# Performance work log

Measured on AMD Instinct MI355X. Metric: run time of the kernel, lower is better.

Reference implementation:

```python
import jax, jax.numpy as jnp
import numpy as np

Q, N, S, A, E, H = 2048, 64, 128, 4, 128, 8
D = E // H
NEG = -1e9

def _mlp(x, w1, b1, w2, b2):
    return jax.nn.silu(x @ w1 + b1) @ w2 + b2

def _mha(x, wq, bq, wk, bk, wv, bv, wo, bo):
    # MultiHeadAttention with default activation=relu applied to q,k,v and output
    q = jax.nn.relu(x @ wq + bq)
    k = jax.nn.relu(x @ wk + bk)
    v = jax.nn.relu(x @ wv + bv)
    def split(t):
        return t.reshape(Q, N, H, D).transpose(0, 2, 1, 3)  # [Q,H,N,D]
    qh, kh, vh = split(q), split(k), split(v)
    scores = jnp.einsum('bhqd,bhkd->bhqk', qh, kh) / (D ** 0.5)
    attn = jax.nn.softmax(scores, axis=-1)
    y = jnp.einsum('bhqk,bhkd->bhqd', attn, vh).transpose(0, 2, 1, 3).reshape(Q, N, E)
    return jax.nn.relu(y @ wo + bo)

def setup_inputs():
    key = jax.random.key(0)
    ks = jax.random.split(key, 26)
    nrm = lambda k, s: jax.random.normal(k, s, jnp.float32) * 0.05
    return {
        'tasks': jax.random.normal(ks[0], (Q, N, N + 4 * S), jnp.float32),
        'constraints': jax.random.normal(ks[1], (Q, A), jnp.float32),
        'masks': jax.random.randint(ks[2], (Q, N, S), 0, 2),
        'topologicals': jax.random.randint(ks[3], (Q, N), 0, N),
        'w_init1': nrm(ks[4], (N + A, 128)), 'b_init1': jnp.zeros((128,), jnp.float32),
        'w_init2': nrm(ks[5], (128, E)), 'b_init2': jnp.zeros((E,), jnp.float32),
        'wq': nrm(ks[6], (E, E)), 'bq': jnp.zeros((E,), jnp.float32),
        'wk': nrm(ks[7], (E, E)), 'bk': jnp.zeros((E,), jnp.float32),
        'wv': nrm(ks[8], (E, E)), 'bv': jnp.zeros((E,), jnp.float32),
        'wo': nrm(ks[9], (E, E)), 'bo': jnp.zeros((E,), jnp.float32),
        'w_node1': nrm(ks[10], (E + A, 128)), 'b_node1': jnp.zeros((128,), jnp.float32),
        'w_node2': nrm(ks[11], (128, E)), 'b_node2': jnp.zeros((E,), jnp.float32),
        'w_ser1': nrm(ks[12], (A, 128)), 'b_ser1': jnp.zeros((128,), jnp.float32),
        'w_ser2': nrm(ks[13], (128, E)), 'b_ser2': jnp.zeros((E,), jnp.float32),
    }

def reference(tasks, constraints, masks, topologicals,
              w_init1, b_init1, w_init2, b_init2,
              wq, bq, wk, bk, wv, bv, wo, bo,
              w_node1, b_node1, w_node2, b_node2,
              w_ser1, b_ser1, w_ser2, b_ser2):
    cons = jnp.broadcast_to(constraints[:, None, :], (Q, N, A))
    node_emb = _mlp(jnp.concatenate([tasks[:, :, :N], cons], -1), w_init1, b_init1, w_init2, b_init2)
    nodes_emb = _mha(node_emb, wq, bq, wk, bk, wv, bv, wo, bo) + node_emb
    # original sets channel 0 to -3 then overwrites with 3; channel 2 stays 0 (kept faithfully)
    qos = jnp.zeros((Q, N, A), jnp.float32).at[:, :, 0].set(3.0).at[:, :, 1].set(1.0).at[:, :, 3].set(1.0)
    ava = jnp.ones((Q,), jnp.float32)
    tp = jnp.full((Q,), 3.0, jnp.float32)
    rel = jnp.ones((Q,), jnp.float32)
    ridx = jnp.zeros((Q, N), jnp.float32)
    rprob = jnp.zeros((Q, N), jnp.float32)
    qidx = jnp.arange(Q)
    topo_seq = topologicals[:, ::-1].T  # [N, Q]: reversed topological order, one node per step
    keys = jax.random.split(jax.random.key(1), N)

    def step(carry, xs):
        qos, ava, tp, rel, ridx, rprob = carry
        topo, k = xs
        task = tasks[qidx, topo]                 # [Q, N + 4S] per-query gathered row
        workflow = task[:, :N]
        response_time = jnp.max(workflow * qos[:, :, 0], axis=1)  # [Q]
        qos_feat = jnp.stack([response_time, ava, tp, rel], axis=-1)
        node_e = nodes_emb[qidx, topo]           # [Q, E]
        tne = _mlp(jnp.concatenate([node_e, qos_feat], -1), w_node1, b_node1, w_node2, b_node2)
        services = task[:, N:].reshape(Q, S, A)
        ser_emb = _mlp(services, w_ser1, b_ser1, w_ser2, b_ser2)
        logits = jnp.einsum('qse,qe->qs', ser_emb, tne)
        mask = masks[qidx, topo]                 # [Q, S]
        logits = jnp.where(mask == 0, NEG, logits)
        ser_prob = jax.nn.softmax(logits, axis=-1)
        ser_idx = jax.random.categorical(k, logits)  # ~ Categorical(ser_prob)
        onehot = jax.nn.one_hot(topo, N, dtype=jnp.float32)
        ridx = ridx + onehot * ser_idx[:, None].astype(jnp.float32)
        rprob = rprob + onehot * ser_prob[qidx, ser_idx][:, None]
        base = ser_idx * 4 + N
        ser_rt = task[qidx, base]
        ser_ava = task[qidx, base + 1]
        ser_tp = task[qidx, base + 2]
        ser_rel = task[qidx, base + 3]
        new_tp = jnp.minimum(ser_tp, tp)
        qos = qos.at[qidx, topo, 0].set(ser_rt + response_time)
        qos = qos.at[qidx, topo, 1].set(ser_ava * ava)
        qos = qos.at[qidx, topo, 2].set(new_tp)
        qos = qos.at[qidx, topo, 3].set(ser_rel * rel)
        return (qos, ser_ava * ava, new_tp, ser_rel * rel, ridx, rprob), None

    (qos, ava, tp, rel, ridx, rprob), _ = jax.lax.scan(
        step, (qos, ava, tp, rel, ridx, rprob), (topo_seq, keys))
    return ridx.astype(jnp.int16), rprob
```

## Files before the change

### kernel.cpp

```cpp
#include <hip/hip_runtime.h>
#include <math.h>

#define Qn 2048
#define Nn 64
#define Sn 128
#define An 4
#define En 128
#define TASKW 576
#define NEGV -1000000000.0f

typedef float v2f __attribute__((ext_vector_type(2)));
typedef float v4f __attribute__((ext_vector_type(4)));

__device__ __forceinline__ v2f mkv2(float a, float b) {
  v2f r; r.x = a; r.y = b; return r;
}
__device__ __forceinline__ v2f lo2(v4f v) { v2f r; r.x = v.x; r.y = v.y; return r; }
__device__ __forceinline__ v2f hi2(v4f v) { v2f r; r.x = v.z; r.y = v.w; return r; }
__device__ __forceinline__ void pkfma(v2f& d, v2f a, v2f b) {
  asm("v_pk_fma_f32 %0, %1, %2, %0" : "+v"(d) : "v"(a), "v"(b));
}
__device__ __forceinline__ v2f pkadd(v2f a, v2f b) {
  v2f d; asm("v_pk_add_f32 %0, %1, %2" : "=v"(d) : "v"(a), "v"(b)); return d;
}

__device__ __forceinline__ void threefry2x32(unsigned k0, unsigned k1,
                                             unsigned x0, unsigned x1,
                                             unsigned& o0, unsigned& o1) {
  unsigned ks2 = k0 ^ k1 ^ 0x1BD11BDAu;
  x0 += k0; x1 += k1;
#define TFR(r) { x0 += x1; x1 = (x1 << (r)) | (x1 >> (32 - (r))); x1 ^= x0; }
  TFR(13) TFR(15) TFR(26) TFR(6)
  x0 += k1;  x1 += ks2 + 1u;
  TFR(17) TFR(29) TFR(16) TFR(24)
  x0 += ks2; x1 += k0 + 2u;
  TFR(13) TFR(15) TFR(26) TFR(6)
  x0 += k0;  x1 += k1 + 3u;
  TFR(17) TFR(29) TFR(16) TFR(24)
  x0 += k1;  x1 += ks2 + 4u;
  TFR(13) TFR(15) TFR(26) TFR(6)
  x0 += ks2; x1 += k0 + 5u;
#undef TFR
  o0 = x0; o1 = x1;
}

__device__ __forceinline__ float silu_f(float x) {
  return x / (1.0f + expf(-x));
}
__device__ __forceinline__ float fexp(float x) {
  return __builtin_amdgcn_exp2f(x * 1.44269504088896f);
}
__device__ __forceinline__ float fsilu(float x) {
  const float e = __builtin_amdgcn_exp2f(x * -1.44269504088896f);
  return x * __builtin_amdgcn_rcpf(1.0f + e);
}
__device__ __forceinline__ float flog(float x) {
  return __builtin_amdgcn_logf(x) * 0.69314718055995f;
}

__global__ void setup_kernel(const float* __restrict__ w_node2,
                             const float* __restrict__ b_node2,
                             const float* __restrict__ w_ser2,
                             const float* __restrict__ b_ser2,
                             float* __restrict__ Mbuf, float* __restrict__ dvec,
                             unsigned* __restrict__ keys) {
  const int b = blockIdx.x, t = threadIdx.x;
  if (b < 128) {
    float acc = 0.0f;
    for (int e = 0; e < 128; ++e)
      acc = fmaf(w_node2[b * 128 + e], w_ser2[t * 128 + e], acc);
    Mbuf[b * 128 + t] = acc;
  } else if (b == 128) {
    float acc = 0.0f;
    for (int e = 0; e < 128; ++e)
      acc = fmaf(b_node2[e], w_ser2[t * 128 + e], acc);
    dvec[t] = acc;
  } else {
    if (t < 64) {
      unsigned o0, o1;
      threefry2x32(0u, 1u, 0u, (unsigned)t, o0, o1);
      keys[2 * t + 0] = o0;
      keys[2 * t + 1] = o1;
    }
  }
}

__global__ __launch_bounds__(256, 2)
void init_mlp_kernel(const float* __restrict__ tasks,
                     const float* __restrict__ cons,
                     const float* __restrict__ w1, const float* __restrict__ b1,
                     const float* __restrict__ w2, const float* __restrict__ b2,
                     float* __restrict__ node_emb) {
  const int q = blockIdx.x, tid = threadIdx.x;
  const int lane = tid & 127, half = tid >> 7;
  __shared__ __align__(16) float xr[2][68];
  __shared__ __align__(16) float sgb[2][128];
  v2f w1p[34], w2p[64];
#pragma unroll
  for (int i = 0; i < 34; ++i)
    w1p[i] = mkv2(w1[(2 * i) * 128 + lane], w1[(2 * i + 1) * 128 + lane]);
#pragma unroll
  for (int j = 0; j < 64; ++j)
    w2p[j] = mkv2(w2[(2 * j) * 128 + lane], w2[(2 * j + 1) * 128 + lane]);
  const float bb1 = b1[lane], bb2 = b2[lane];
  for (int r = 0; r < 64; r += 2) {
    if (tid < 136) {
      const int rr = tid / 68, j = tid - rr * 68;
      xr[rr][j] = (j < 64) ? tasks[(q * 64 + r + rr) * TASKW + j]
                           : cons[q * 4 + (j - 64)];
    }
    __syncthreads();
    v2f gp = mkv2(0.0f, 0.0f);
    const v4f* xr4 = (const v4f*)&xr[half][0];
#pragma unroll
    for (int i = 0; i < 17; ++i) {
      const v4f x = xr4[i];
      pkfma(gp, lo2(x), w1p[2 * i]);
      pkfma(gp, hi2(x), w1p[2 * i + 1]);
    }
    const float g = gp.x + gp.y + bb1;
    sgb[half][lane] = silu_f(g);
    __syncthreads();
    v2f op = mkv2(0.0f, 0.0f);
    const v4f* sgb4 = (const v4f*)&sgb[half][0];
#pragma unroll
    for (int j = 0; j < 32; ++j) {
      const v4f s = sgb4[j];
      pkfma(op, lo2(s), w2p[2 * j]);
      pkfma(op, hi2(s), w2p[2 * j + 1]);
    }
    node_emb[(q * 64 + r + half) * 128 + lane] = op.x + op.y + bb2;
    __syncthreads();
  }
}

__global__ __launch_bounds__(256, 2)
void mha_kernel(const float* __restrict__ node_emb,
                const float* __restrict__ wq, const float* __restrict__ bq,
                const float* __restrict__ wk, const float* __restrict__ bk,
                const float* __restrict__ wv, const float* __restrict__ bv,
                float* __restrict__ y_out) {
  const int q = blockIdx.x, tid = threadIdx.x;
  __shared__ __align__(16) float xs[64][132];
  __shared__ __align__(16) float qh[64][20];
  __shared__ __align__(16) float kh[64][20];
  __shared__ __align__(16) float vt[16][68];
  __shared__ __align__(16) float pool[3 * 16 * 132];
  float (*wht)[16][132] = (float (*)[16][132])pool;
  float (*at)[68] = (float (*)[68])pool;

  for (int idx = tid; idx < 64 * 32; idx += 256) {
    const int n = idx >> 5, e4 = idx & 31;
    *(v4f*)&xs[n][4 * e4] =
        *(const v4f*)&node_emb[(q * 64 + n) * 128 + 4 * e4];
  }
  __syncthreads();

  const int d16 = tid >> 4;
  const int ng = tid & 15;

  for (int hd = 0; hd < 8; ++hd) {
    for (int idx = tid; idx < 3 * 128 * 16; idx += 256) {
      const int m = idx >> 11, k = (idx >> 4) & 127, d = idx & 15;
      const float* W = (m == 0) ? wq : (m == 1) ? wk : wv;
      wht[m][d][k] = W[k * 128 + hd * 16 + d];
    }
    __syncthreads();

    {
      const float bqv = bq[hd * 16 + d16];
      const float bkv = bk[hd * 16 + d16];
      const float bvv = bv[hd * 16 + d16];
      const v4f* wq4 = (const v4f*)&wht[0][d16][0];
      const v4f* wk4 = (const v4f*)&wht[1][d16][0];
      const v4f* wv4 = (const v4f*)&wht[2][d16][0];
      const v4f* xr0 = (const v4f*)&xs[ng][0];
      const v4f* xr1 = (const v4f*)&xs[ng + 16][0];
      const v4f* xr2 = (const v4f*)&xs[ng + 32][0];
      const v4f* xr3 = (const v4f*)&xs[ng + 48][0];
      v2f aq0 = mkv2(0, 0), aq1 = mkv2(0, 0), aq2 = mkv2(0, 0), aq3 = mkv2(0, 0);
      v2f ak0 = mkv2(0, 0), ak1 = mkv2(0, 0), ak2 = mkv2(0, 0), ak3 = mkv2(0, 0);
      v2f av0 = mkv2(0, 0), av1 = mkv2(0, 0), av2 = mkv2(0, 0), av3 = mkv2(0, 0);
#pragma unroll 4
      for (int kk = 0; kk < 32; ++kk) {
        const v4f wqv = wq4[kk], wkv = wk4[kk], wvv = wv4[kk];
        const v4f x0 = xr0[kk], x1 = xr1[kk], x2 = xr2[kk], x3 = xr3[kk];
        const v2f wqa = lo2(wqv), wqb = hi2(wqv);
        const v2f wka = lo2(wkv), wkb = hi2(wkv);
        const v2f wva = lo2(wvv), wvb = hi2(wvv);
        const v2f x0a = lo2(x0), x0b = hi2(x0);
        const v2f x1a = lo2(x1), x1b = hi2(x1);
        const v2f x2a = lo2(x2), x2b = hi2(x2);
        const v2f x3a = lo2(x3), x3b = hi2(x3);
        pkfma(aq0, x0a, wqa); pkfma(aq0, x0b, wqb);
        pkfma(aq1, x1a, wqa); pkfma(aq1, x1b, wqb);
        pkfma(aq2, x2a, wqa); pkfma(aq2, x2b, wqb);
        pkfma(aq3, x3a, wqa); pkfma(aq3, x3b, wqb);
        pkfma(ak0, x0a, wka); pkfma(ak0, x0b, wkb);
        pkfma(ak1, x1a, wka); pkfma(ak1, x1b, wkb);
        pkfma(ak2, x2a, wka); pkfma(ak2, x2b, wkb);
        pkfma(ak3, x3a, wka); pkfma(ak3, x3b, wkb);
        pkfma(av0, x0a, wva); pkfma(av0, x0b, wvb);
        pkfma(av1, x1a, wva); pkfma(av1, x1b, wvb);
        pkfma(av2, x2a, wva); pkfma(av2, x2b, wvb);
        pkfma(av3, x3a, wva); pkfma(av3, x3b, wvb);
      }
      qh[ng][d16] = fmaxf(aq0.x + aq0.y + bqv, 0.0f);
      qh[ng + 16][d16] = fmaxf(aq1.x + aq1.y + bqv, 0.0f);
      qh[ng + 32][d16] = fmaxf(aq2.x + aq2.y + bqv, 0.0f);
      qh[ng + 48][d16] = fmaxf(aq3.x + aq3.y + bqv, 0.0f);
      kh[ng][d16] = fmaxf(ak0.x + ak0.y + bkv, 0.0f);
      kh[ng + 16][d16] = fmaxf(ak1.x + ak1.y + bkv, 0.0f);
      kh[ng + 32][d16] = fmaxf(ak2.x + ak2.y + bkv, 0.0f);
      kh[ng + 48][d16] = fmaxf(ak3.x + ak3.y + bkv, 0.0f);
      vt[d16][ng] = fmaxf(av0.x + av0.y + bvv, 0.0f);
      vt[d16][ng + 16] = fmaxf(av1.x + av1.y + bvv, 0.0f);
      vt[d16][ng + 32] = fmaxf(av2.x + av2.y + bvv, 0.0f);
      vt[d16][ng + 48] = fmaxf(av3.x + av3.y + bvv, 0.0f);
    }
    __syncthreads();

    {
      const int n = tid >> 2, mg = tid & 3;
      v4f qv[4];
      const v4f* qrow = (const v4f*)&qh[n][0];
#pragma unroll
      for (int kk = 0; kk < 4; ++kk) qv[kk] = qrow[kk];
#pragma unroll 4
      for (int jj = 0; jj < 16; ++jj) {
        const int m = mg + 4 * jj;
        const v4f* krow = (const v4f*)&kh[m][0];
        v2f accp = mkv2(0.0f, 0.0f);
#pragma unroll
        for (int kk = 0; kk < 4; ++kk) {
          const v4f kv = krow[kk];
          pkfma(accp, lo2(qv[kk]), lo2(kv));
          pkfma(accp, hi2(qv[kk]), hi2(kv));
        }
        at[n][m] = (accp.x + accp.y) * 0.25f;
      }
    }
    __syncthreads();

    {
      const int r = tid >> 2, p = tid & 3;
      const v4f* arow = (const v4f*)&at[r][p * 16];
      v4f av[4];
#pragma unroll
      for (int u = 0; u < 4; ++u) av[u] = arow[u];
      float mx = -1e30f;
#pragma unroll
      for (int u = 0; u < 4; ++u) {
        mx = fmaxf(mx, fmaxf(fmaxf(av[u].x, av[u].y), fmaxf(av[u].z, av[u].w)));
      }
      mx = fmaxf(mx, __shfl_xor(mx, 1, 64));
      mx = fmaxf(mx, __shfl_xor(mx, 2, 64));
      float s = 0.0f;
#pragma unroll
      for (int u = 0; u < 4; ++u) {
        av[u].x = fexp(av[u].x - mx); av[u].y = fexp(av[u].y - mx);
        av[u].z = fexp(av[u].z - mx); av[u].w = fexp(av[u].w - mx);
        s += av[u].x + av[u].y + av[u].z + av[u].w;
      }
      s += __shfl_xor(s, 1, 64);
      s += __shfl_xor(s, 2, 64);
      const float rs = __builtin_amdgcn_rcpf(s);
      v4f* wrow = (v4f*)&at[r][p * 16];
#pragma unroll
      for (int u = 0; u < 4; ++u) {
        av[u].x *= rs; av[u].y *= rs; av[u].z *= rs; av[u].w *= rs;
        wrow[u] = av[u];
      }
    }
    __syncthreads();

    {
      const int dd = tid & 15, ngr = tid >> 4;
      const v4f* vrow = (const v4f*)&vt[dd][0];
      const v4f* ar0 = (const v4f*)&at[ngr][0];
      const v4f* ar1 = (const v4f*)&at[ngr + 16][0];
      const v4f* ar2 = (const v4f*)&at[ngr + 32][0];
      const v4f* ar3 = (const v4f*)&at[ngr + 48][0];
      v2f ac0 = mkv2(0, 0), ac1 = mkv2(0, 0), ac2 = mkv2(0, 0), ac3 = mkv2(0, 0);
#pragma unroll 4
      for (int kk = 0; kk < 16; ++kk) {
        const v4f vv = vrow[kk];
        const v2f va = lo2(vv), vb = hi2(vv);
        const v4f a0 = ar0[kk], a1 = ar1[kk], a2 = ar2[kk], a3 = ar3[kk];
        pkfma(ac0, lo2(a0), va); pkfma(ac0, hi2(a0), vb);
        pkfma(ac1, lo2(a1), va); pkfma(ac1, hi2(a1), vb);
        pkfma(ac2, lo2(a2), va); pkfma(ac2, hi2(a2), vb);
        pkfma(ac3, lo2(a3), va); pkfma(ac3, hi2(a3), vb);
      }
      y_out[(q * 64 + ngr) * 128 + hd * 16 + dd] = ac0.x + ac0.y;
      y_out[(q * 64 + ngr + 16) * 128 + hd * 16 + dd] = ac1.x + ac1.y;
      y_out[(q * 64 + ngr + 32) * 128 + hd * 16 + dd] = ac2.x + ac2.y;
      y_out[(q * 64 + ngr + 48) * 128 + hd * 16 + dd] = ac3.x + ac3.y;
    }
    __syncthreads();
  }
}

__global__ __launch_bounds__(256, 2)
void outgb_kernel(const float* __restrict__ resid, const float* __restrict__ y,
                  const float* __restrict__ wo, const float* __restrict__ bo,
                  const float* __restrict__ w_node1,
                  const float* __restrict__ b_node1,
                  float* __restrict__ gbase) {
  const int q = blockIdx.x, tid = threadIdx.x;
  __shared__ __align__(16) float ys[64][132];
  __shared__ __align__(16) float wot[32][132];
  for (int idx = tid; idx < 64 * 32; idx += 256) {
    const int n = idx >> 5, e4 = idx & 31;
    *(v4f*)&ys[n][4 * e4] = *(const v4f*)&y[(q * 64 + n) * 128 + 4 * e4];
  }
  const int cg = tid & 15, ngr = tid >> 4;
  float nodes[4][8];

#pragma unroll
  for (int tile = 0; tile < 4; ++tile) {
    const int c0 = 32 * tile;
    __syncthreads();
    for (int idx = tid; idx < 32 * 128; idx += 256) {
      const int k = idx >> 5, c = idx & 31;
      wot[c][k] = wo[k * 128 + c0 + c];
    }
    __syncthreads();
    const int c = c0 + 2 * cg;
    const v4f* w0 = (const v4f*)&wot[2 * cg][0];
    const v4f* w1 = (const v4f*)&wot[2 * cg + 1][0];
    const v4f* yr0 = (const v4f*)&ys[ngr][0];
    const v4f* yr1 = (const v4f*)&ys[ngr + 16][0];
    const v4f* yr2 = (const v4f*)&ys[ngr + 32][0];
    const v4f* yr3 = (const v4f*)&ys[ngr + 48][0];
    v2f a00 = mkv2(0, 0), a01 = mkv2(0, 0), a10 = mkv2(0, 0), a11 = mkv2(0, 0);
    v2f a20 = mkv2(0, 0), a21 = mkv2(0, 0), a30 = mkv2(0, 0), a31 = mkv2(0, 0);
#pragma unroll 4
    for (int kk = 0; kk < 32; ++kk) {
      const v4f wv0 = w0[kk], wv1 = w1[kk];
      const v2f w0a = lo2(wv0), w0b = hi2(wv0);
      const v2f w1a = lo2(wv1), w1b = hi2(wv1);
      const v4f x0 = yr0[kk], x1 = yr1[kk], x2 = yr2[kk], x3 = yr3[kk];
      pkfma(a00, lo2(x0), w0a); pkfma(a00, hi2(x0), w0b);
      pkfma(a01, lo2(x0), w1a); pkfma(a01, hi2(x0), w1b);
      pkfma(a10, lo2(x1), w0a); pkfma(a10, hi2(x1), w0b);
      pkfma(a11, lo2(x1), w1a); pkfma(a11, hi2(x1), w1b);
      pkfma(a20, lo2(x2), w0a); pkfma(a20, hi2(x2), w0b);
      pkfma(a21, lo2(x2), w1a); pkfma(a21, hi2(x2), w1b);
      pkfma(a30, lo2(x3), w0a); pkfma(a30, hi2(x3), w0b);
      pkfma(a31, lo2(x3), w1a); pkfma(a31, hi2(x3), w1b);
    }
    const float b0v = bo[c], b1v = bo[c + 1];
#define PROJ_EMIT(J, A0, A1)                                                  \
    {                                                                         \
      const int n = ngr + 16 * J;                                             \
      const float2 res = *(const float2*)&resid[(q * 64 + n) * 128 + c];      \
      nodes[J][2 * tile] = fmaxf(A0.x + A0.y + b0v, 0.0f) + res.x;            \
      nodes[J][2 * tile + 1] = fmaxf(A1.x + A1.y + b1v, 0.0f) + res.y;        \
    }
    PROJ_EMIT(0, a00, a01)
    PROJ_EMIT(1, a10, a11)
    PROJ_EMIT(2, a20, a21)
    PROJ_EMIT(3, a30, a31)
#undef PROJ_EMIT
  }
  __syncthreads();
#pragma unroll
  for (int j = 0; j < 4; ++j) {
    const int n = ngr + 16 * j;
#pragma unroll
    for (int tile = 0; tile < 4; ++tile) {
      *(float2*)&ys[n][32 * tile + 2 * cg] =
          make_float2(nodes[j][2 * tile], nodes[j][2 * tile + 1]);
    }
  }

#pragma unroll
  for (int tile = 0; tile < 4; ++tile) {
    const int c0 = 32 * tile;
    __syncthreads();
    for (int idx = tid; idx < 32 * 128; idx += 256) {
      const int k = idx >> 5, c = idx & 31;
      wot[c][k] = w_node1[k * 128 + c0 + c];
    }
    __syncthreads();
    const int c = c0 + 2 * cg;
    const v4f* w0 = (const v4f*)&wot[2 * cg][0];
    const v4f* w1 = (const v4f*)&wot[2 * cg + 1][0];
    const v4f* yr0 = (const v4f*)&ys[ngr][0];
    const v4f* yr1 = (const v4f*)&ys[ngr + 16][0];
    const v4f* yr2 = (const v4f*)&ys[ngr + 32][0];
    const v4f* yr3 = (const v4f*)&ys[ngr + 48][0];
    v2f a00 = mkv2(0, 0), a01 = mkv2(0, 0), a10 = mkv2(0, 0), a11 = mkv2(0, 0);
    v2f a20 = mkv2(0, 0), a21 = mkv2(0, 0), a30 = mkv2(0, 0), a31 = mkv2(0, 0);
#pragma unroll 4
    for (int kk = 0; kk < 32; ++kk) {
      const v4f wv0 = w0[kk], wv1 = w1[kk];
      const v2f w0a = lo2(wv0), w0b = hi2(wv0);
      const v2f w1a = lo2(wv1), w1b = hi2(wv1);
      const v4f x0 = yr0[kk], x1 = yr1[kk], x2 = yr2[kk], x3 = yr3[kk];
      pkfma(a00, lo2(x0), w0a); pkfma(a00, hi2(x0), w0b);
      pkfma(a01, lo2(x0), w1a); pkfma(a01, hi2(x0), w1b);
      pkfma(a10, lo2(x1), w0a); pkfma(a10, hi2(x1), w0b);
      pkfma(a11, lo2(x1), w1a); pkfma(a11, hi2(x1), w1b);
      pkfma(a20, lo2(x2), w0a); pkfma(a20, hi2(x2), w0b);
      pkfma(a21, lo2(x2), w1a); pkfma(a21, hi2(x2), w1b);
      pkfma(a30, lo2(x3), w0a); pkfma(a30, hi2(x3), w0b);
      pkfma(a31, lo2(x3), w1a); pkfma(a31, hi2(x3), w1b);
    }
    const float b0v = b_node1[c], b1v = b_node1[c + 1];
#define GB_EMIT(J, A0, A1)                                                    \
    {                                                                         \
      const int n = ngr + 16 * J;                                             \
      float2 o;                                                               \
      o.x = A0.x + A0.y + b0v;                                                \
      o.y = A1.x + A1.y + b1v;                                                \
      *(float2*)&gbase[(q * 64 + n) * 128 + c] = o;                           \
    }
    GB_EMIT(0, a00, a01)
    GB_EMIT(1, a10, a11)
    GB_EMIT(2, a20, a21)
    GB_EMIT(3, a30, a31)
#undef GB_EMIT
  }
}

__global__ __launch_bounds__(256, 3)
void scan_kernel(const float* __restrict__ tasks, const int* __restrict__ masks,
                 const int* __restrict__ topologicals,
                 const float* __restrict__ w_node1,
                 const float* __restrict__ w_ser1,
                 const float* __restrict__ b_ser1,
                 const float* __restrict__ gbase,
                 const float* __restrict__ Mbuf, const float* __restrict__ dvec,
                 const unsigned* __restrict__ keys, float* __restrict__ out) {
  const int q = blockIdx.x, tid = threadIdx.x;
  const int lane = tid & 127, half = tid >> 7;
  const int wl = tid & 63;
  const int wave = tid >> 6;

  __shared__ __align__(16) float task_s[2][TASKW];
  __shared__ __align__(16) float gb_s[2][128];
  __shared__ int mask_s[2][128];
  __shared__ int topo_s[64];
  __shared__ __align__(16) float sg[128];
  __shared__ __align__(16) v2f wfull_s[64][6];
  __shared__ __align__(16) float red[256];
  __shared__ float lcomp_s[128];
  __shared__ float gla_s[128];
  __shared__ int act_s[128];
  __shared__ float qr_s[64];
  __shared__ float ridx_s[64], rprob_s[64];
  __shared__ __align__(16) v4f qw4_s[128];
  __shared__ __align__(16) float dvs[128];
  __shared__ unsigned keys_s[128];
  __shared__ int na_s;

  v2f Mr2[32];
#pragma unroll
  for (int j = 0; j < 32; ++j)
    Mr2[j] = mkv2(Mbuf[(half * 64 + 2 * j) * 128 + lane],
                  Mbuf[(half * 64 + 2 * j + 1) * 128 + lane]);

  if (tid < 64) {
    topo_s[tid] = topologicals[q * 64 + tid];
    const int j = tid;
#pragma unroll
    for (int c = 0; c < 4; ++c)
      wfull_s[j][c] =
          mkv2(w_ser1[c * 128 + 2 * j], w_ser1[c * 128 + 2 * j + 1]);
    wfull_s[j][4] = mkv2(b_ser1[2 * j], b_ser1[2 * j + 1]);
    qr_s[tid] = 3.0f;
    ridx_s[tid] = 0.0f;
    rprob_s[tid] = 0.0f;
  }
  if (tid < 128) {
    dvs[tid] = dvec[tid];
    keys_s[tid] = keys[tid];
    v4f qp;
    qp.x = w_node1[128 * 128 + tid];
    qp.y = w_node1[129 * 128 + tid];
    qp.z = w_node1[130 * 128 + tid];
    qp.w = w_node1[131 * 128 + tid];
    qw4_s[tid] = qp;
  }
  float ava = 1.0f, tp = 3.0f, rel = 1.0f;
  __syncthreads();

  {
    const int topo0 = topo_s[63];
    if (tid < 144)
      ((float4*)task_s[0])[tid] =
          ((const float4*)(tasks + (size_t)(q * 64 + topo0) * TASKW))[tid];
    if (tid < 128) {
      gb_s[0][tid] = gbase[(q * 64 + topo0) * 128 + tid];
      mask_s[0][tid] = masks[(q * 64 + topo0) * 128 + tid];
    }
  }
  __syncthreads();

  for (int t = 0; t < 64; ++t) {
    const int cur = t & 1, nxt = cur ^ 1;
    const int topo = topo_s[63 - t];

    float rt = 0.0f;
    if (wave < 2) {
      float p = task_s[cur][wl] * qr_s[wl];
#pragma unroll
      for (int o = 32; o > 0; o >>= 1) p = fmaxf(p, __shfl_xor(p, o, 64));
      rt = p;
    } else if (wave == 2) {
      const int m0 = mask_s[cur][wl] != 0;
      const int m1 = mask_s[cur][wl + 64] != 0;
      const unsigned long long b0 = __ballot(m0);
      const unsigned long long b1 = __ballot(m1);
      const unsigned long long lt = (1ull << wl) - 1ull;
      const int c0 = __popcll(b0);
      if (m0) act_s[__popcll(b0 & lt)] = wl;
      if (m1) act_s[c0 + __popcll(b1 & lt)] = wl + 64;
      if (wl == 0) na_s = c0 + __popcll(b1);
    }
    if (tid < 128) {
      const v4f qp = qw4_s[tid];
      float g = gb_s[cur][tid];
      g = fmaf(rt, qp.x, g);
      g = fmaf(ava, qp.y, g);
      g = fmaf(tp, qp.z, g);
      g = fmaf(rel, qp.w, g);
      sg[tid] = fsilu(g);
    }
    __syncthreads();
    const int na = na_s;

    {
      v2f accp = mkv2(0.0f, 0.0f);
      const v4f* sgp = (const v4f*)sg + half * 16;
#pragma unroll
      for (int j = 0; j < 16; ++j) {
        const v4f x = sgp[j];
        pkfma(accp, lo2(x), Mr2[2 * j]);
        pkfma(accp, hi2(x), Mr2[2 * j + 1]);
      }
      red[tid] = accp.x + accp.y;
    }
    __syncthreads();
    if (tid < 64) {
      const v2f r0 = *(const v2f*)&red[2 * tid];
      const v2f r1 = *(const v2f*)&red[2 * tid + 128];
      const v2f dv = *(const v2f*)&dvs[2 * tid];
      wfull_s[tid][5] = pkadd(pkadd(r0, r1), dv);
    }
    __syncthreads();

    float4 pf_task;
    float pf_gb;
    int pf_mask;
    {
      const int tn = (t < 63) ? t + 1 : 63;
      const int ntopo = topo_s[63 - tn];
      if (tid < 144)
        pf_task =
            ((const float4*)(tasks + (size_t)(q * 64 + ntopo) * TASKW))[tid];
      if (tid < 128) {
        pf_gb = gbase[(q * 64 + ntopo) * 128 + tid];
        pf_mask = masks[(q * 64 + ntopo) * 128 + tid];
      }
    }

    {
      const int g8 = tid >> 3, o = tid & 7;
      const int sl0 = 4 * g8;
      if (wave * 32 < na) {
        const int s0 = (sl0 + 0 < na) ? act_s[sl0 + 0] : 0;
        const int s1 = (sl0 + 1 < na) ? act_s[sl0 + 1] : 0;
        const int s2 = (sl0 + 2 < na) ? act_s[sl0 + 2] : 0;
        const int s3 = (sl0 + 3 < na) ? act_s[sl0 + 3] : 0;
        const float4 svA = *(const float4*)&task_s[cur][64 + 4 * s0];
        const float4 svB = *(const float4*)&task_s[cur][64 + 4 * s1];
        const float4 svC = *(const float4*)&task_s[cur][64 + 4 * s2];
        const float4 svD = *(const float4*)&task_s[cur][64 + 4 * s3];
        const v2f A0 = mkv2(svA.x, svA.x), A1 = mkv2(svA.y, svA.y),
                  A2 = mkv2(svA.z, svA.z), A3 = mkv2(svA.w, svA.w);
        const v2f B0 = mkv2(svB.x, svB.x), B1 = mkv2(svB.y, svB.y),
                  B2 = mkv2(svB.z, svB.z), B3 = mkv2(svB.w, svB.w);
        const v2f C0 = mkv2(svC.x, svC.x), C1 = mkv2(svC.y, svC.y),
                  C2 = mkv2(svC.z, svC.z), C3 = mkv2(svC.w, svC.w);
        const v2f D0 = mkv2(svD.x, svD.x), D1 = mkv2(svD.y, svD.y),
                  D2 = mkv2(svD.z, svD.z), D3 = mkv2(svD.w, svD.w);
        v2f ac0 = mkv2(0, 0), ac1 = mkv2(0, 0), ac2 = mkv2(0, 0),
            ac3 = mkv2(0, 0);
        const v4f* wp = (const v4f*)&wfull_s[0][0];
#pragma unroll
        for (int jj = 0; jj < 8; ++jj) {
          const int j = o + 8 * jj;
          const v4f wA = wp[3 * j], wB = wp[3 * j + 1], wC = wp[3 * j + 2];
          const v2f w0 = lo2(wA), w1 = hi2(wA);
          const v2f w2 = lo2(wB), w3 = hi2(wB);
          const v2f bp = lo2(wC), up = hi2(wC);
#define SRV(AC, X0, X1, X2, X3)                                               \
          {                                                                   \
            v2f p = bp;                                                       \
            pkfma(p, X0, w0); pkfma(p, X1, w1);                               \
            pkfma(p, X2, w2); pkfma(p, X3, w3);                               \
            const float ex =                                                  \
                __builtin_amdgcn_exp2f(p.x * -1.44269504088896f);             \
            const float ey =                                                  \
                __builtin_amdgcn_exp2f(p.y * -1.44269504088896f);             \
            const float rx = __builtin_amdgcn_rcpf(1.0f + ex);                \
            const float ry = __builtin_amdgcn_rcpf(1.0f + ey);                \
            pkfma(AC, mkv2(p.x * rx, p.y * ry), up);                          \
          }
          SRV(ac0, A0, A1, A2, A3)
          SRV(ac1, B0, B1, B2, B3)
          SRV(ac2, C0, C1, C2, C3)
          SRV(ac3, D0, D1, D2, D3)
#undef SRV
        }
        float l0 = ac0.x + ac0.y, l1 = ac1.x + ac1.y;
        float l2 = ac2.x + ac2.y, l3 = ac3.x + ac3.y;
        l0 += __shfl_xor(l0, 1, 64); l0 += __shfl_xor(l0, 2, 64);
        l0 += __shfl_xor(l0, 4, 64);
        l1 += __shfl_xor(l1, 1, 64); l1 += __shfl_xor(l1, 2, 64);
        l1 += __shfl_xor(l1, 4, 64);
        l2 += __shfl_xor(l2, 1, 64); l2 += __shfl_xor(l2, 2, 64);
        l2 += __shfl_xor(l2, 4, 64);
        l3 += __shfl_xor(l3, 1, 64); l3 += __shfl_xor(l3, 2, 64);
        l3 += __shfl_xor(l3, 4, 64);
        if (o == 0) {
          if (sl0 + 3 < na) {
            *(float4*)&lcomp_s[sl0] = make_float4(l0, l1, l2, l3);
          } else {
            if (sl0 + 0 < na) lcomp_s[sl0 + 0] = l0;
            if (sl0 + 1 < na) lcomp_s[sl0 + 1] = l1;
            if (sl0 + 2 < na) lcomp_s[sl0 + 2] = l2;
          }
        }
      }
    }
    __syncthreads();

    if (tid < 128) {
      float gv = -3.0e38f;
      if (tid < na) {
        const int s = act_s[tid];
        unsigned o0, o1;
        threefry2x32(keys_s[2 * t], keys_s[2 * t + 1], 0u,
                     (unsigned)(q * 128 + s), o0, o1);
        const unsigned bits = o0 ^ o1;
        const float f = __uint_as_float((bits >> 9) | 0x3f800000u) - 1.0f;
        const float u = (f > 0.0f) ? f : 1.17549435e-38f;
        gv = lcomp_s[tid] - flog(-flog(u));
      }
      gla_s[tid] = gv;
    }
    if (tid < 144) ((float4*)task_s[nxt])[tid] = pf_task;
    if (tid < 128) {
      gb_s[nxt][tid] = pf_gb;
      mask_s[nxt][tid] = pf_mask;
    }
    __syncthreads();

    int si, kstar;
    {
      float z = gla_s[wl];
      int zi = wl;
      const float z2 = gla_s[wl + 64];
      if (z2 > z) { z = z2; zi = wl + 64; }
#pragma unroll
      for (int o = 32; o > 0; o >>= 1) {
        const float zo = __shfl_xor(z, o, 64);
        const int io = __shfl_xor(zi, o, 64);
        if (zo > z || (zo == z && io < zi)) { z = zo; zi = io; }
      }
      kstar = zi;
      si = act_s[zi];
    }
    if (wave == 3) {
      const float la = (wl < na) ? lcomp_s[wl] : -3.0e38f;
      const float lb = (wl + 64 < na) ? lcomp_s[wl + 64] : -3.0e38f;
      float mx = fmaxf(la, lb);
#pragma unroll
      for (int o = 32; o > 0; o >>= 1) mx = fmaxf(mx, __shfl_xor(mx, o, 64));
      float e = fexp(la - mx) + fexp(lb - mx);
#pragma unroll
      for (int o = 32; o > 0; o >>= 1) e += __shfl_xor(e, o, 64);
      if (wl == 0)
        rprob_s[topo] += fexp(lcomp_s[kstar] - mx) * __builtin_amdgcn_rcpf(e);
    }
    {
      const float s1v = task_s[cur][64 + 4 * si + 1];
      const float s2v = task_s[cur][64 + 4 * si + 2];
      const float s3v = task_s[cur][64 + 4 * si + 3];
      if (tid == 0) {
        const float s0v = task_s[cur][64 + 4 * si];
        qr_s[topo] = s0v + rt;
        ridx_s[topo] += (float)si;
      }
      ava = s1v * ava;
      tp = fminf(s2v, tp);
      rel = s3v * rel;
    }
    __syncthreads();
  }
  if (tid < 64) {
    out[q * 64 + tid] = ridx_s[tid];
    out[Qn * Nn + q * 64 + tid] = rprob_s[tid];
  }
}

extern "C" void kernel_launch(void* const* d_in, const int* in_sizes, int n_in,
                              void* d_out, int out_size, void* d_ws,
                              size_t ws_size, hipStream_t stream) {
  const float* tasks = (const float*)d_in[0];
  const float* constraints = (const float*)d_in[1];
  const int* masks = (const int*)d_in[2];
  const int* topologicals = (const int*)d_in[3];
  const float* w_init1 = (const float*)d_in[4];
  const float* b_init1 = (const float*)d_in[5];
  const float* w_init2 = (const float*)d_in[6];
  const float* b_init2 = (const float*)d_in[7];
  const float* wq = (const float*)d_in[8];
  const float* bq = (const float*)d_in[9];
  const float* wk = (const float*)d_in[10];
  const float* bk = (const float*)d_in[11];
  const float* wv = (const float*)d_in[12];
  const float* bv = (const float*)d_in[13];
  const float* wo = (const float*)d_in[14];
  const float* bo = (const float*)d_in[15];
  const float* w_node1 = (const float*)d_in[16];
  const float* b_node1 = (const float*)d_in[17];
  const float* w_node2 = (const float*)d_in[18];
  const float* b_node2 = (const float*)d_in[19];
  const float* w_ser1 = (const float*)d_in[20];
  const float* b_ser1 = (const float*)d_in[21];
  const float* w_ser2 = (const float*)d_in[22];
  const float* b_ser2 = (const float*)d_in[23];

  float* ws = (float*)d_ws;
  float* node_emb = ws;
  float* ybuf = node_emb + (size_t)Qn * Nn * En;
  float* Mbuf = ybuf + (size_t)Qn * Nn * En;
  float* dvec = Mbuf + 128 * 128;
  unsigned* keys = (unsigned*)(dvec + 128);
  float* gbase = node_emb;

  setup_kernel<<<130, 128, 0, stream>>>(w_node2, b_node2, w_ser2, b_ser2, Mbuf,
                                        dvec, keys);
  init_mlp_kernel<<<Qn, 256, 0, stream>>>(tasks, constraints, w_init1, b_init1,
                                          w_init2, b_init2, node_emb);
  mha_kernel<<<Qn, 256, 0, stream>>>(node_emb, wq, bq, wk, bk, wv, bv, ybuf);
  outgb_kernel<<<Qn, 256, 0, stream>>>(node_emb, ybuf, wo, bo, w_node1,
                                       b_node1, gbase);
  scan_kernel<<<Qn, 256, 0, stream>>>(tasks, masks, topologicals, w_node1,
                                      w_ser1, b_ser1, gbase, Mbuf, dvec, keys,
                                      (float*)d_out);
}
```

Baseline: 2.069 ms.

## Restructure scan step to cut barriers and stream M matrix from cache

The per-step scan loop is reorganised to use fewer block barriers. Waves 0-1 compute the gated embedding and 128x128 projection directly, with M re-laid out as interleaved float4 and read from global/L2 instead of held in 64 registers per thread. Waves 2-3 compute the Gumbel noise and prefetch the next step's data at the same time. The logit MLP uses op_sel broadcast packed FMAs with 16-lane groups. Freeing the registers lets launch bounds rise to 6 blocks per SM, at the cost of re-reading M from cache every step.

```diff
diff --git a/kernel.cpp b/kernel.cpp
--- a/kernel.cpp
+++ b/kernel.cpp
@@ -20,8 +20,13 @@
 __device__ __forceinline__ void pkfma(v2f& d, v2f a, v2f b) {
   asm("v_pk_fma_f32 %0, %1, %2, %0" : "+v"(d) : "v"(a), "v"(b));
 }
-__device__ __forceinline__ v2f pkadd(v2f a, v2f b) {
-  v2f d; asm("v_pk_add_f32 %0, %1, %2" : "=v"(d) : "v"(a), "v"(b)); return d;
+__device__ __forceinline__ void pkfma_bl(v2f& d, v2f a, v2f b) {
+  asm("v_pk_fma_f32 %0, %1, %2, %0 op_sel:[0,0,0] op_sel_hi:[0,1,1]"
+      : "+v"(d) : "v"(a), "v"(b));
+}
+__device__ __forceinline__ void pkfma_bh(v2f& d, v2f a, v2f b) {
+  asm("v_pk_fma_f32 %0, %1, %2, %0 op_sel:[1,0,0] op_sel_hi:[1,1,1]"
+      : "+v"(d) : "v"(a), "v"(b));
 }
 
 __device__ __forceinline__ void threefry2x32(unsigned k0, unsigned k1,
@@ -62,14 +67,14 @@
                              const float* __restrict__ b_node2,
                              const float* __restrict__ w_ser2,
                              const float* __restrict__ b_ser2,
-                             float* __restrict__ Mbuf, float* __restrict__ dvec,
+                             float* __restrict__ Mt4, float* __restrict__ dvec,
                              unsigned* __restrict__ keys) {
   const int b = blockIdx.x, t = threadIdx.x;
   if (b < 128) {
     float acc = 0.0f;
     for (int e = 0; e < 128; ++e)
       acc = fmaf(w_node2[b * 128 + e], w_ser2[t * 128 + e], acc);
-    Mbuf[b * 128 + t] = acc;
+    Mt4[(((b >> 2) * 128) + t) * 4 + (b & 3)] = acc;
   } else if (b == 128) {
     float acc = 0.0f;
     for (int e = 0; e < 128; ++e)
@@ -425,64 +430,60 @@
   }
 }
 
-__global__ __launch_bounds__(256, 3)
+__global__ __launch_bounds__(256, 6)
 void scan_kernel(const float* __restrict__ tasks, const int* __restrict__ masks,
                  const int* __restrict__ topologicals,
                  const float* __restrict__ w_node1,
                  const float* __restrict__ w_ser1,
                  const float* __restrict__ b_ser1,
                  const float* __restrict__ gbase,
-                 const float* __restrict__ Mbuf, const float* __restrict__ dvec,
+                 const float* __restrict__ Mt4, const float* __restrict__ dvec,
                  const unsigned* __restrict__ keys, float* __restrict__ out) {
   const int q = blockIdx.x, tid = threadIdx.x;
-  const int lane = tid & 127, half = tid >> 7;
-  const int wl = tid & 63;
-  const int wave = tid >> 6;
+  const int wl = tid & 63, wave = tid >> 6;
+  const int g16 = tid >> 4, oo = tid & 15;
 
   __shared__ __align__(16) float task_s[2][TASKW];
   __shared__ __align__(16) float gb_s[2][128];
   __shared__ int mask_s[2][128];
   __shared__ int topo_s[64];
   __shared__ __align__(16) float sg[128];
-  __shared__ __align__(16) v2f wfull_s[64][6];
-  __shared__ __align__(16) float red[256];
+  __shared__ __align__(16) v4f wa_s[64];
+  __shared__ __align__(16) v4f wb_s[64];
+  __shared__ __align__(16) v2f bp_s[64];
+  __shared__ __align__(16) v2f up_s[64];
+  __shared__ float gn_s[128];
   __shared__ float lcomp_s[128];
-  __shared__ float gla_s[128];
   __shared__ int act_s[128];
   __shared__ float qr_s[64];
   __shared__ float ridx_s[64], rprob_s[64];
-  __shared__ __align__(16) v4f qw4_s[128];
-  __shared__ __align__(16) float dvs[128];
   __shared__ unsigned keys_s[128];
   __shared__ int na_s;
-
-  v2f Mr2[32];
-#pragma unroll
-  for (int j = 0; j < 32; ++j)
-    Mr2[j] = mkv2(Mbuf[(half * 64 + 2 * j) * 128 + lane],
-                  Mbuf[(half * 64 + 2 * j + 1) * 128 + lane]);
 
   if (tid < 64) {
     topo_s[tid] = topologicals[q * 64 + tid];
     const int j = tid;
-#pragma unroll
-    for (int c = 0; c < 4; ++c)
-      wfull_s[j][c] =
-          mkv2(w_ser1[c * 128 + 2 * j], w_ser1[c * 128 + 2 * j + 1]);
-    wfull_s[j][4] = mkv2(b_ser1[2 * j], b_ser1[2 * j + 1]);
+    v4f wa, wb;
+    wa.x = w_ser1[0 * 128 + 2 * j]; wa.y = w_ser1[0 * 128 + 2 * j + 1];
+    wa.z = w_ser1[1 * 128 + 2 * j]; wa.w = w_ser1[1 * 128 + 2 * j + 1];
+    wb.x = w_ser1[2 * 128 + 2 * j]; wb.y = w_ser1[2 * 128 + 2 * j + 1];
+    wb.z = w_ser1[3 * 128 + 2 * j]; wb.w = w_ser1[3 * 128 + 2 * j + 1];
+    wa_s[j] = wa;
+    wb_s[j] = wb;
+    bp_s[j] = mkv2(b_ser1[2 * j], b_ser1[2 * j + 1]);
     qr_s[tid] = 3.0f;
     ridx_s[tid] = 0.0f;
     rprob_s[tid] = 0.0f;
   }
+  float dv_r = 0.0f;
+  v4f qp_r; qp_r.x = 0; qp_r.y = 0; qp_r.z = 0; qp_r.w = 0;
   if (tid < 128) {
-    dvs[tid] = dvec[tid];
     keys_s[tid] = keys[tid];
-    v4f qp;
-    qp.x = w_node1[128 * 128 + tid];
-    qp.y = w_node1[129 * 128 + tid];
-    qp.z = w_node1[130 * 128 + tid];
-    qp.w = w_node1[131 * 128 + tid];
-    qw4_s[tid] = qp;
+    dv_r = dvec[tid];
+    qp_r.x = w_node1[128 * 128 + tid];
+    qp_r.y = w_node1[129 * 128 + tid];
+    qp_r.z = w_node1[130 * 128 + tid];
+    qp_r.w = w_node1[131 * 128 + tid];
   }
   float ava = 1.0f, tp = 3.0f, rel = 1.0f;
   __syncthreads();
@@ -502,14 +503,29 @@
   for (int t = 0; t < 64; ++t) {
     const int cur = t & 1, nxt = cur ^ 1;
     const int topo = topo_s[63 - t];
+    const int tn = (t < 63) ? t + 1 : 63;
+    const int ntopo = topo_s[63 - tn];
 
     float rt = 0.0f;
+    float4 pf_t[3];
+    float pf_g0 = 0.0f, pf_g1 = 0.0f;
+    int pf_m0 = 0, pf_m1 = 0;
     if (wave < 2) {
       float p = task_s[cur][wl] * qr_s[wl];
 #pragma unroll
       for (int o = 32; o > 0; o >>= 1) p = fmaxf(p, __shfl_xor(p, o, 64));
       rt = p;
+      float g = gb_s[cur][tid];
+      g = fmaf(rt, qp_r.x, g);
+      g = fmaf(ava, qp_r.y, g);
+      g = fmaf(tp, qp_r.z, g);
+      g = fmaf(rel, qp_r.w, g);
+      sg[tid] = fsilu(g);
     } else if (wave == 2) {
+      pf_g0 = gbase[(q * 64 + ntopo) * 128 + wl];
+      pf_g1 = gbase[(q * 64 + ntopo) * 128 + wl + 64];
+      pf_m0 = masks[(q * 64 + ntopo) * 128 + wl];
+      pf_m1 = masks[(q * 64 + ntopo) * 128 + wl + 64];
       const int m0 = mask_s[cur][wl] != 0;
       const int m1 = mask_s[cur][wl + 64] != 0;
       const unsigned long long b0 = __ballot(m0);
@@ -519,173 +535,145 @@
       if (m0) act_s[__popcll(b0 & lt)] = wl;
       if (m1) act_s[c0 + __popcll(b1 & lt)] = wl + 64;
       if (wl == 0) na_s = c0 + __popcll(b1);
-    }
+    } else {
+#pragma unroll
+      for (int r = 0; r < 3; ++r) {
+        const int idx = wl + 64 * r;
+        if (idx < 144)
+          pf_t[r] =
+              ((const float4*)(tasks + (size_t)(q * 64 + ntopo) * TASKW))[idx];
+      }
+    }
+    __syncthreads();
+    const int na = na_s;
+
     if (tid < 128) {
-      const v4f qp = qw4_s[tid];
-      float g = gb_s[cur][tid];
-      g = fmaf(rt, qp.x, g);
-      g = fmaf(ava, qp.y, g);
-      g = fmaf(tp, qp.z, g);
-      g = fmaf(rel, qp.w, g);
-      sg[tid] = fsilu(g);
-    }
-    __syncthreads();
-    const int na = na_s;
-
-    {
-      v2f accp = mkv2(0.0f, 0.0f);
-      const v4f* sgp = (const v4f*)sg + half * 16;
-#pragma unroll
-      for (int j = 0; j < 16; ++j) {
-        const v4f x = sgp[j];
-        pkfma(accp, lo2(x), Mr2[2 * j]);
-        pkfma(accp, hi2(x), Mr2[2 * j + 1]);
-      }
-      red[tid] = accp.x + accp.y;
-    }
-    __syncthreads();
-    if (tid < 64) {
-      const v2f r0 = *(const v2f*)&red[2 * tid];
-      const v2f r1 = *(const v2f*)&red[2 * tid + 128];
-      const v2f dv = *(const v2f*)&dvs[2 * tid];
-      wfull_s[tid][5] = pkadd(pkadd(r0, r1), dv);
-    }
-    __syncthreads();
-
-    float4 pf_task;
-    float pf_gb;
-    int pf_mask;
-    {
-      const int tn = (t < 63) ? t + 1 : 63;
-      const int ntopo = topo_s[63 - tn];
-      if (tid < 144)
-        pf_task =
-            ((const float4*)(tasks + (size_t)(q * 64 + ntopo) * TASKW))[tid];
-      if (tid < 128) {
-        pf_gb = gbase[(q * 64 + ntopo) * 128 + tid];
-        pf_mask = masks[(q * 64 + ntopo) * 128 + tid];
-      }
-    }
-
-    {
-      const int g8 = tid >> 3, o = tid & 7;
-      const int sl0 = 4 * g8;
-      if (wave * 32 < na) {
-        const int s0 = (sl0 + 0 < na) ? act_s[sl0 + 0] : 0;
-        const int s1 = (sl0 + 1 < na) ? act_s[sl0 + 1] : 0;
-        const int s2 = (sl0 + 2 < na) ? act_s[sl0 + 2] : 0;
-        const int s3 = (sl0 + 3 < na) ? act_s[sl0 + 3] : 0;
-        const float4 svA = *(const float4*)&task_s[cur][64 + 4 * s0];
-        const float4 svB = *(const float4*)&task_s[cur][64 + 4 * s1];
-        const float4 svC = *(const float4*)&task_s[cur][64 + 4 * s2];
-        const float4 svD = *(const float4*)&task_s[cur][64 + 4 * s3];
-        const v2f A0 = mkv2(svA.x, svA.x), A1 = mkv2(svA.y, svA.y),
-                  A2 = mkv2(svA.z, svA.z), A3 = mkv2(svA.w, svA.w);
-        const v2f B0 = mkv2(svB.x, svB.x), B1 = mkv2(svB.y, svB.y),
-                  B2 = mkv2(svB.z, svB.z), B3 = mkv2(svB.w, svB.w);
-        const v2f C0 = mkv2(svC.x, svC.x), C1 = mkv2(svC.y, svC.y),
-                  C2 = mkv2(svC.z, svC.z), C3 = mkv2(svC.w, svC.w);
-        const v2f D0 = mkv2(svD.x, svD.x), D1 = mkv2(svD.y, svD.y),
-                  D2 = mkv2(svD.z, svD.z), D3 = mkv2(svD.w, svD.w);
-        v2f ac0 = mkv2(0, 0), ac1 = mkv2(0, 0), ac2 = mkv2(0, 0),
-            ac3 = mkv2(0, 0);
-        const v4f* wp = (const v4f*)&wfull_s[0][0];
-#pragma unroll
-        for (int jj = 0; jj < 8; ++jj) {
-          const int j = o + 8 * jj;
-          const v4f wA = wp[3 * j], wB = wp[3 * j + 1], wC = wp[3 * j + 2];
-          const v2f w0 = lo2(wA), w1 = hi2(wA);
-          const v2f w2 = lo2(wB), w3 = hi2(wB);
-          const v2f bp = lo2(wC), up = hi2(wC);
-#define SRV(AC, X0, X1, X2, X3)                                               \
-          {                                                                   \
-            v2f p = bp;                                                       \
-            pkfma(p, X0, w0); pkfma(p, X1, w1);                               \
-            pkfma(p, X2, w2); pkfma(p, X3, w3);                               \
-            const float ex =                                                  \
-                __builtin_amdgcn_exp2f(p.x * -1.44269504088896f);             \
-            const float ey =                                                  \
-                __builtin_amdgcn_exp2f(p.y * -1.44269504088896f);             \
-            const float rx = __builtin_amdgcn_rcpf(1.0f + ex);                \
-            const float ry = __builtin_amdgcn_rcpf(1.0f + ey);                \
-            pkfma(AC, mkv2(p.x * rx, p.y * ry), up);                          \
-          }
-          SRV(ac0, A0, A1, A2, A3)
-          SRV(ac1, B0, B1, B2, B3)
-          SRV(ac2, C0, C1, C2, C3)
-          SRV(ac3, D0, D1, D2, D3)
-#undef SRV
-        }
-        float l0 = ac0.x + ac0.y, l1 = ac1.x + ac1.y;
-        float l2 = ac2.x + ac2.y, l3 = ac3.x + ac3.y;
-        l0 += __shfl_xor(l0, 1, 64); l0 += __shfl_xor(l0, 2, 64);
-        l0 += __shfl_xor(l0, 4, 64);
-        l1 += __shfl_xor(l1, 1, 64); l1 += __shfl_xor(l1, 2, 64);
-        l1 += __shfl_xor(l1, 4, 64);
-        l2 += __shfl_xor(l2, 1, 64); l2 += __shfl_xor(l2, 2, 64);
-        l2 += __shfl_xor(l2, 4, 64);
-        l3 += __shfl_xor(l3, 1, 64); l3 += __shfl_xor(l3, 2, 64);
-        l3 += __shfl_xor(l3, 4, 64);
-        if (o == 0) {
-          if (sl0 + 3 < na) {
-            *(float4*)&lcomp_s[sl0] = make_float4(l0, l1, l2, l3);
-          } else {
-            if (sl0 + 0 < na) lcomp_s[sl0 + 0] = l0;
-            if (sl0 + 1 < na) lcomp_s[sl0 + 1] = l1;
-            if (sl0 + 2 < na) lcomp_s[sl0 + 2] = l2;
-          }
-        }
-      }
-    }
-    __syncthreads();
-
-    if (tid < 128) {
-      float gv = -3.0e38f;
-      if (tid < na) {
-        const int s = act_s[tid];
+      v2f a0 = mkv2(0.0f, 0.0f), a1 = mkv2(0.0f, 0.0f);
+      const v4f* Mg = ((const v4f*)Mt4) + tid;
+      const v4f* sg4 = (const v4f*)sg;
+#pragma unroll 8
+      for (int j4 = 0; j4 < 32; ++j4) {
+        const v4f m = Mg[j4 * 128];
+        const v4f s = sg4[j4];
+        pkfma(a0, lo2(s), lo2(m));
+        pkfma(a1, hi2(s), hi2(m));
+      }
+      const float u = a0.x + a0.y + a1.x + a1.y + dv_r;
+      const float u2 = __shfl_xor(u, 1, 64);
+      if ((tid & 1) == 0) up_s[tid >> 1] = mkv2(u, u2);
+    } else {
+      const int slot = tid - 128;
+      if (slot < na) {
+        const int s = act_s[slot];
         unsigned o0, o1;
         threefry2x32(keys_s[2 * t], keys_s[2 * t + 1], 0u,
                      (unsigned)(q * 128 + s), o0, o1);
         const unsigned bits = o0 ^ o1;
         const float f = __uint_as_float((bits >> 9) | 0x3f800000u) - 1.0f;
-        const float u = (f > 0.0f) ? f : 1.17549435e-38f;
-        gv = lcomp_s[tid] - flog(-flog(u));
-      }
-      gla_s[tid] = gv;
-    }
-    if (tid < 144) ((float4*)task_s[nxt])[tid] = pf_task;
-    if (tid < 128) {
-      gb_s[nxt][tid] = pf_gb;
-      mask_s[nxt][tid] = pf_mask;
-    }
-    __syncthreads();
-
-    int si, kstar;
-    {
-      float z = gla_s[wl];
-      int zi = wl;
-      const float z2 = gla_s[wl + 64];
-      if (z2 > z) { z = z2; zi = wl + 64; }
-#pragma unroll
-      for (int o = 32; o > 0; o >>= 1) {
-        const float zo = __shfl_xor(z, o, 64);
-        const int io = __shfl_xor(zi, o, 64);
-        if (zo > z || (zo == z && io < zi)) { z = zo; zi = io; }
-      }
-      kstar = zi;
-      si = act_s[zi];
-    }
+        const float uu = (f > 0.0f) ? f : 1.17549435e-38f;
+        gn_s[slot] = -flog(-flog(uu));
+      }
+    }
+    __syncthreads();
+
     if (wave == 3) {
-      const float la = (wl < na) ? lcomp_s[wl] : -3.0e38f;
-      const float lb = (wl + 64 < na) ? lcomp_s[wl + 64] : -3.0e38f;
-      float mx = fmaxf(la, lb);
+#pragma unroll
+      for (int r = 0; r < 3; ++r) {
+        const int idx = wl + 64 * r;
+        if (idx < 144) ((float4*)task_s[nxt])[idx] = pf_t[r];
+      }
+    } else if (wave == 2) {
+      gb_s[nxt][wl] = pf_g0;
+      gb_s[nxt][wl + 64] = pf_g1;
+      mask_s[nxt][wl] = pf_m0;
+      mask_s[nxt][wl + 64] = pf_m1;
+    }
+
+    auto logits_block = [&](const int sl0) {
+      const int s0 = (sl0 + 0 < na) ? act_s[sl0 + 0] : 0;
+      const int s1 = (sl0 + 1 < na) ? act_s[sl0 + 1] : 0;
+      const int s2 = (sl0 + 2 < na) ? act_s[sl0 + 2] : 0;
+      const int s3 = (sl0 + 3 < na) ? act_s[sl0 + 3] : 0;
+      const v4f svA = *(const v4f*)&task_s[cur][64 + 4 * s0];
+      const v4f svB = *(const v4f*)&task_s[cur][64 + 4 * s1];
+      const v4f svC = *(const v4f*)&task_s[cur][64 + 4 * s2];
+      const v4f svD = *(const v4f*)&task_s[cur][64 + 4 * s3];
+      v2f ac0 = mkv2(0.0f, 0.0f), ac1 = mkv2(0.0f, 0.0f);
+      v2f ac2 = mkv2(0.0f, 0.0f), ac3 = mkv2(0.0f, 0.0f);
+#pragma unroll
+      for (int jj = 0; jj < 4; ++jj) {
+        const int j = oo + 16 * jj;
+        const v4f wA = wa_s[j];
+        const v4f wB = wb_s[j];
+        const v2f bp = bp_s[j];
+        const v2f up = up_s[j];
+#define SRV(AC, SV)                                                           \
+        {                                                                     \
+          v2f p = bp;                                                         \
+          pkfma_bl(p, lo2(SV), lo2(wA));                                      \
+          pkfma_bh(p, lo2(SV), hi2(wA));                                      \
+          pkfma_bl(p, hi2(SV), lo2(wB));                                      \
+          pkfma_bh(p, hi2(SV), hi2(wB));                                      \
+          const float ex = __builtin_amdgcn_exp2f(p.x * -1.44269504088896f);  \
+          const float ey = __builtin_amdgcn_exp2f(p.y * -1.44269504088896f);  \
+          const float rx = __builtin_amdgcn_rcpf(1.0f + ex);                  \
+          const float ry = __builtin_amdgcn_rcpf(1.0f + ey);                  \
+          pkfma(AC, mkv2(p.x * rx, p.y * ry), up);                            \
+        }
+        SRV(ac0, svA)
+        SRV(ac1, svB)
+        SRV(ac2, svC)
+        SRV(ac3, svD)
+#undef SRV
+      }
+      float l0 = ac0.x + ac0.y, l1 = ac1.x + ac1.y;
+      float l2 = ac2.x + ac2.y, l3 = ac3.x + ac3.y;
+      l0 += __shfl_xor(l0, 1, 64); l0 += __shfl_xor(l0, 2, 64);
+      l0 += __shfl_xor(l0, 4, 64); l0 += __shfl_xor(l0, 8, 64);
+      l1 += __shfl_xor(l1, 1, 64); l1 += __shfl_xor(l1, 2, 64);
+      l1 += __shfl_xor(l1, 4, 64); l1 += __shfl_xor(l1, 8, 64);
+      l2 += __shfl_xor(l2, 1, 64); l2 += __shfl_xor(l2, 2, 64);
+      l2 += __shfl_xor(l2, 4, 64); l2 += __shfl_xor(l2, 8, 64);
+      l3 += __shfl_xor(l3, 1, 64); l3 += __shfl_xor(l3, 2, 64);
+      l3 += __shfl_xor(l3, 4, 64); l3 += __shfl_xor(l3, 8, 64);
+      if (oo == 0) {
+        if (sl0 + 3 < na) {
+          *(float4*)&lcomp_s[sl0] = make_float4(l0, l1, l2, l3);
+        } else {
+          if (sl0 + 0 < na) lcomp_s[sl0 + 0] = l0;
+          if (sl0 + 1 < na) lcomp_s[sl0 + 1] = l1;
+          if (sl0 + 2 < na) lcomp_s[sl0 + 2] = l2;
+        }
+      }
+    };
+    if (16 * wave < na) logits_block(4 * g16);
+    if (64 + 16 * wave < na) logits_block(64 + 4 * g16);
+    __syncthreads();
+
+    float la = -3.0e38f, lb = -3.0e38f;
+    if (wl < na) la = lcomp_s[wl] + gn_s[wl];
+    if (wl + 64 < na) lb = lcomp_s[wl + 64] + gn_s[wl + 64];
+    float z = la;
+    int zi = wl;
+    if (lb > z) { z = lb; zi = wl + 64; }
+#pragma unroll
+    for (int o = 32; o > 0; o >>= 1) {
+      const float zo = __shfl_xor(z, o, 64);
+      const int io = __shfl_xor(zi, o, 64);
+      if (zo > z || (zo == z && io < zi)) { z = zo; zi = io; }
+    }
+    const int si = act_s[zi];
+    if (wave == 3) {
+      const float ma = (wl < na) ? lcomp_s[wl] : -3.0e38f;
+      const float mb = (wl + 64 < na) ? lcomp_s[wl + 64] : -3.0e38f;
+      float mx = fmaxf(ma, mb);
 #pragma unroll
       for (int o = 32; o > 0; o >>= 1) mx = fmaxf(mx, __shfl_xor(mx, o, 64));
-      float e = fexp(la - mx) + fexp(lb - mx);
+      float e = fexp(ma - mx) + fexp(mb - mx);
 #pragma unroll
       for (int o = 32; o > 0; o >>= 1) e += __shfl_xor(e, o, 64);
       if (wl == 0)
-        rprob_s[topo] += fexp(lcomp_s[kstar] - mx) * __builtin_amdgcn_rcpf(e);
+        rprob_s[topo] += fexp(lcomp_s[zi] - mx) * __builtin_amdgcn_rcpf(e);
     }
     {
       const float s1v = task_s[cur][64 + 4 * si + 1];
@@ -739,12 +727,12 @@
   float* ws = (float*)d_ws;
   float* node_emb = ws;
   float* ybuf = node_emb + (size_t)Qn * Nn * En;
-  float* Mbuf = ybuf + (size_t)Qn * Nn * En;
-  float* dvec = Mbuf + 128 * 128;
+  float* Mt4 = ybuf + (size_t)Qn * Nn * En;
+  float* dvec = Mt4 + 128 * 128;
   unsigned* keys = (unsigned*)(dvec + 128);
   float* gbase = node_emb;
 
-  setup_kernel<<<130, 128, 0, stream>>>(w_node2, b_node2, w_ser2, b_ser2, Mbuf,
+  setup_kernel<<<130, 128, 0, stream>>>(w_node2, b_node2, w_ser2, b_ser2, Mt4,
                                         dvec, keys);
   init_mlp_kernel<<<Qn, 256, 0, stream>>>(tasks, constraints, w_init1, b_init1,
                                           w_init2, b_init2, node_emb);
@@ -752,6 +740,6 @@
   outgb_kernel<<<Qn, 256, 0, stream>>>(node_emb, ybuf, wo, bo, w_node1,
                                        b_node1, gbase);
   scan_kernel<<<Qn, 256, 0, stream>>>(tasks, masks, topologicals, w_node1,
-                                      w_ser1, b_ser1, gbase, Mbuf, dvec, keys,
+                                      w_ser1, b_ser1, gbase, Mt4, dvec, keys,
                                       (float*)d_out);
 }
```

New measurement: 2.327 ms. 12.5% more time.
